# Performance work log

Hardware: AMD Instinct MI355X
Metric: run time of the kernel (lower is better)

Reference implementation:

```python
import jax, jax.numpy as jnp
import numpy as np

LOSS_ALPHA = 0.7  # Config.loss_alpha


def setup_inputs() -> dict:
    key = jax.random.key(0)
    k1, k2, k3 = jax.random.split(key, 3)
    N, D, K = 1024, 256, 65536
    online_emb = jax.random.normal(k1, (N, D), dtype=jnp.float32)
    mom_emb = jax.random.normal(k2, (N, D), dtype=jnp.float32)
    queue = jax.random.normal(k3, (D, K), dtype=jnp.float32)
    temp = jnp.full((1,), 0.07, dtype=jnp.float32)
    return {"online_emb": online_emb, "mom_emb": mom_emb, "queue": queue, "temp": temp}


def _ce_label0(logits):
    # cross-entropy with target class 0 for every row, mean over batch
    return jnp.mean(jax.nn.logsumexp(logits, axis=1) - logits[:, 0])


def reference(online_emb, mom_emb, queue, temp):
    pos_sim = jnp.einsum('nd,nd->n', online_emb, mom_emb)          # [N]
    neg_sim = jnp.einsum('nd,dk->nk', online_emb, queue)           # [N, K]
    logits_raw = jnp.concatenate([pos_sim[:, None], neg_sim], axis=1)  # [N, K+1]
    t = temp[0]
    loss_online = _ce_label0(logits_raw / t)
    loss_momentum = _ce_label0(logits_raw / jax.lax.stop_gradient(t))
    return LOSS_ALPHA * loss_online + (1.0 - LOSS_ALPHA) * loss_momentum
```

## Files before the change

### kernel.cpp

```cpp
#include <hip/hip_runtime.h>
#include <hip/hip_bf16.h>


#define NROWS 1024
#define DDIM  256
#define KQ    65536
#define BN    128
#define NPART 512
#define LN2_F 0.69314718055994531f

typedef short  short8  __attribute__((ext_vector_type(8)));
typedef float  floatx4 __attribute__((ext_vector_type(4)));

__device__ __forceinline__ unsigned short f2bf(float f) {
    unsigned int u = __float_as_uint(f);
    u += 0x7FFFu + ((u >> 16) & 1u);
    return (unsigned short)(u >> 16);
}

#define DPPMOV(x, ctrl) \
    __uint_as_float(__builtin_amdgcn_mov_dpp(__float_as_uint(x), (ctrl), 0xF, 0xF, true))

__device__ __forceinline__ float dpp16_max(float x) {
    x = fmaxf(x, DPPMOV(x, 0xB1));
    x = fmaxf(x, DPPMOV(x, 0x4E));
    x = fmaxf(x, DPPMOV(x, 0x141));
    x = fmaxf(x, DPPMOV(x, 0x140));
    return x;
}
__device__ __forceinline__ float dpp16_sum(float x) {
    x += DPPMOV(x, 0xB1);
    x += DPPMOV(x, 0x4E);
    x += DPPMOV(x, 0x141);
    x += DPPMOV(x, 0x140);
    return x;
}

__global__ __launch_bounds__(256)
void conv_a(const float* __restrict__ A, const float* __restrict__ temp,
            unsigned short* __restrict__ Ab, float* __restrict__ out)
{
    if (blockIdx.x == 0 && threadIdx.x == 0) out[0] = 0.0f;
    const float s = 1.0f / (temp[0] * LN2_F);
    const int i = blockIdx.x * 256 + threadIdx.x;
    const floatx4 v = ((const floatx4*)A)[i];
    ushort4 w;
    w.x = f2bf(v.x * s); w.y = f2bf(v.y * s);
    w.z = f2bf(v.z * s); w.w = f2bf(v.w * s);
    ((ushort4*)Ab)[i] = w;
}

__global__ __launch_bounds__(512, 4)
void gemm_softmax(const unsigned short* __restrict__ Ab,
                  const float* __restrict__ Q,
                  float2* __restrict__ partials)
{
    __shared__ __align__(16) unsigned short Bl[BN * DDIM];

    const int tid  = threadIdx.x;
    const int lane = tid & 63;
    const int wave = tid >> 6;
    const int l15  = lane & 15;
    const int quad = lane >> 4;
    const int nb   = blockIdx.x;
    const int nbase = nb * BN;

    #pragma unroll 1
    for (int iter = 0; iter < 2; ++iter) {
        const int t2 = iter * 512 + tid;
        const int ny = t2 & 31;
        const int ko = t2 >> 5;
        floatx4 v[8];
        #pragma unroll
        for (int j = 0; j < 8; ++j)
            v[j] = __builtin_nontemporal_load(
                       (const floatx4*)(Q + (size_t)(ko * 8 + j) * KQ + nbase + ny * 4));
        #pragma unroll
        for (int i2 = 0; i2 < 4; ++i2) {
            const int n = ny * 4 + i2;
            const int phys = ko ^ (n & 15);
            short8 w;
            #pragma unroll
            for (int j = 0; j < 8; ++j)
                w[j] = (short)f2bf(v[j][i2]);
            *(short8*)&Bl[n * DDIM + phys * 8] = w;
        }
    }
    __syncthreads();

    #pragma unroll 1
    for (int g = 0; g < 4; ++g) {
        const int rowbase = g * 256 + wave * 32;
        const unsigned short* apb = Ab + (size_t)(rowbase + l15) * DDIM + quad * 8;

        floatx4 acc[2][8] = {};
        short8 af[2], bf[8];

        #pragma unroll 1
        for (int s = 0; s < 8; ++s) {
            #pragma unroll
            for (int i = 0; i < 2; ++i)
                af[i] = *(const short8*)(apb + i * 16 * DDIM + s * 32);
            {
                const int vb = l15 * 512 + (((4 * s + quad) ^ l15) * 16);
                #pragma unroll
                for (int j = 0; j < 8; ++j)
                    bf[j] = *(const short8*)((const char*)Bl + vb + j * 8192);
            }
            __builtin_amdgcn_s_setprio(1);
            #pragma unroll
            for (int i = 0; i < 2; ++i)
                #pragma unroll
                for (int j = 0; j < 8; ++j)
                    acc[i][j] = __builtin_amdgcn_mfma_f32_16x16x32_bf16(af[i], bf[j], acc[i][j], 0, 0, 0);
            __builtin_amdgcn_s_setprio(0);
        }

        #pragma unroll
        for (int i = 0; i < 2; ++i) {
            float2 tmp[4];
            #pragma unroll
            for (int r = 0; r < 4; ++r) {
                float mx = acc[i][0][r];
                #pragma unroll
                for (int j = 1; j < 8; ++j) mx = fmaxf(mx, acc[i][j][r]);
                mx = dpp16_max(mx);
                float s2 = 0.f;
                #pragma unroll
                for (int j = 0; j < 8; ++j)
                    s2 += __builtin_amdgcn_exp2f(acc[i][j][r] - mx);
                s2 = dpp16_sum(s2);
                tmp[r] = make_float2(mx, s2);
            }
            if (l15 == 0) {
                const int row = rowbase + i * 16 + quad * 4;
                floatx4* dst = (floatx4*)(partials + (size_t)nb * NROWS + row);
                floatx4 w0 = {tmp[0].x, tmp[0].y, tmp[1].x, tmp[1].y};
                floatx4 w1 = {tmp[2].x, tmp[2].y, tmp[3].x, tmp[3].y};
                __builtin_nontemporal_store(w0, dst);
                __builtin_nontemporal_store(w1, dst + 1);
            }
        }
    }
}

__global__ __launch_bounds__(256)
void finalize_rows(const float2* __restrict__ partials,
                   const float* __restrict__ online,
                   const float* __restrict__ mom,
                   const float* __restrict__ temp,
                   float* __restrict__ out)
{
    const int t = threadIdx.x;
    __shared__ float2 sm[16][17];
    __shared__ float sm_pos[16];

    {
        const float s = 1.0f / (temp[0] * LN2_F);
        const int r2 = t >> 4, c2 = t & 15;
        const float* po = online + (size_t)(blockIdx.x * 16 + r2) * DDIM + c2 * 16;
        const float* pm = mom    + (size_t)(blockIdx.x * 16 + r2) * DDIM + c2 * 16;
        float d = 0.f;
        #pragma unroll
        for (int w = 0; w < 4; ++w) {
            const floatx4 a = *(const floatx4*)(po + w * 4);
            const floatx4 b = *(const floatx4*)(pm + w * 4);
            d += a.x * b.x + a.y * b.y + a.z * b.z + a.w * b.w;
        }
        d = dpp16_sum(d);
        if (c2 == 0) sm_pos[r2] = d * s;
    }

    const int rl  = t & 15;
    const int grp = t >> 4;
    const int row = blockIdx.x * 16 + rl;

    float M = -3.0e38f, S = 0.f;
    #pragma unroll 1
    for (int pb = 0; pb < 32; pb += 8) {
        float2 v[8];
        #pragma unroll
        for (int j = 0; j < 8; ++j)
            v[j] = partials[(size_t)(grp * 32 + pb + j) * NROWS + row];
        #pragma unroll
        for (int j = 0; j < 8; ++j) {
            const float M2 = fmaxf(M, v[j].x);
            S = S * __builtin_amdgcn_exp2f(M - M2) + v[j].y * __builtin_amdgcn_exp2f(v[j].x - M2);
            M = M2;
        }
    }
    sm[grp][rl] = make_float2(M, S);
    __syncthreads();

    if (t < 64) {
        float val = 0.f;
        if (t < 16) {
            float Mm = -3.0e38f, Ss = 0.f;
            #pragma unroll
            for (int g2 = 0; g2 < 16; ++g2) {
                const float2 v = sm[g2][t];
                const float M2 = fmaxf(Mm, v.x);
                Ss = Ss * __builtin_amdgcn_exp2f(Mm - M2) + v.y * __builtin_amdgcn_exp2f(v.x - M2);
                Mm = M2;
            }
            const float p  = sm_pos[t];
            const float M2 = fmaxf(Mm, p);
            const float L  = Ss * __builtin_amdgcn_exp2f(Mm - M2) + __builtin_amdgcn_exp2f(p - M2);
            val = (M2 + __builtin_amdgcn_logf(L) - p) * LN2_F;
        }
        val += __shfl_xor(val, 1, 64);
        val += __shfl_xor(val, 2, 64);
        val += __shfl_xor(val, 4, 64);
        val += __shfl_xor(val, 8, 64);
        val += __shfl_xor(val, 16, 64);
        val += __shfl_xor(val, 32, 64);
        if (t == 0) atomicAdd(out, val * (1.0f / (float)NROWS));
    }
}

extern "C" void kernel_launch(void* const* d_in, const int* in_sizes, int n_in,
                              void* d_out, int out_size, void* d_ws, size_t ws_size,
                              hipStream_t stream)
{
    const float* online = (const float*)d_in[0];
    const float* mom    = (const float*)d_in[1];
    const float* queue  = (const float*)d_in[2];
    const float* temp   = (const float*)d_in[3];
    float* out = (float*)d_out;

    char* ws = (char*)d_ws;
    unsigned short* Ab = (unsigned short*)ws;
    float2* partials   = (float2*)(ws + 524288);

    conv_a<<<256, 256, 0, stream>>>(online, temp, Ab, out);
    gemm_softmax<<<KQ / BN, 512, 0, stream>>>(Ab, queue, partials);
    finalize_rows<<<64, 256, 0, stream>>>(partials, online, mom, temp, out);
}
```

Baseline: 146.6 us.

## Split queue tile staging into two K-halves to overlap load with MFMA

The B tile in LDS is split into two halves along D. The first half is loaded and converted, and the load of the second half is issued before the first compute pass, then written to LDS after the first half's MFMAs for the first row group. The goal is to hide part of the global load latency of the queue tile behind compute instead of stalling all waves before any MFMA. Holding the second-half registers live during compute raises register pressure. The first row group also takes an extra barrier.

Result: slower. 159.0 us (+8.5%).

```diff
diff --git a/kernel.cpp b/kernel.cpp
--- a/kernel.cpp
+++ b/kernel.cpp
@@ -55,7 +55,7 @@
                   const float* __restrict__ Q,
                   float2* __restrict__ partials)
 {
-    __shared__ __align__(16) unsigned short Bl[BN * DDIM];
+    __shared__ __align__(16) unsigned short Bl[2][BN * 128];
 
     const int tid  = threadIdx.x;
     const int lane = tid & 63;
@@ -65,47 +65,47 @@
     const int nb   = blockIdx.x;
     const int nbase = nb * BN;
 
-    #pragma unroll 1
-    for (int iter = 0; iter < 2; ++iter) {
-        const int t2 = iter * 512 + tid;
-        const int ny = t2 & 31;
-        const int ko = t2 >> 5;
-        floatx4 v[8];
+    const int ny = tid & 31;
+    const int ko = tid >> 5;
+
+    {
+        floatx4 v0[8];
         #pragma unroll
         for (int j = 0; j < 8; ++j)
-            v[j] = __builtin_nontemporal_load(
-                       (const floatx4*)(Q + (size_t)(ko * 8 + j) * KQ + nbase + ny * 4));
+            v0[j] = __builtin_nontemporal_load(
+                        (const floatx4*)(Q + (size_t)(ko * 8 + j) * KQ + nbase + ny * 4));
         #pragma unroll
         for (int i2 = 0; i2 < 4; ++i2) {
             const int n = ny * 4 + i2;
             const int phys = ko ^ (n & 15);
             short8 w;
             #pragma unroll
-            for (int j = 0; j < 8; ++j)
-                w[j] = (short)f2bf(v[j][i2]);
-            *(short8*)&Bl[n * DDIM + phys * 8] = w;
-        }
-    }
-    __syncthreads();
-
-    #pragma unroll 1
-    for (int g = 0; g < 4; ++g) {
-        const int rowbase = g * 256 + wave * 32;
-        const unsigned short* apb = Ab + (size_t)(rowbase + l15) * DDIM + quad * 8;
-
-        floatx4 acc[2][8] = {};
-        short8 af[2], bf[8];
-
+            for (int j = 0; j < 8; ++j) w[j] = (short)f2bf(v0[j][i2]);
+            *(short8*)&Bl[0][n * 128 + phys * 8] = w;
+        }
+    }
+    floatx4 sv[8];
+    #pragma unroll
+    for (int j = 0; j < 8; ++j)
+        sv[j] = __builtin_nontemporal_load(
+                    (const floatx4*)(Q + (size_t)(128 + ko * 8 + j) * KQ + nbase + ny * 4));
+
+    asm volatile("s_waitcnt lgkmcnt(0)" ::: "memory");
+    __builtin_amdgcn_s_barrier();
+
+    auto half_steps = [&](floatx4 (&acc)[2][8], const unsigned short* apb,
+                          const char* blc, int af_off) {
         #pragma unroll 1
-        for (int s = 0; s < 8; ++s) {
+        for (int s = 0; s < 4; ++s) {
+            short8 af[2], bf[8];
             #pragma unroll
             for (int i = 0; i < 2; ++i)
-                af[i] = *(const short8*)(apb + i * 16 * DDIM + s * 32);
+                af[i] = *(const short8*)(apb + i * 16 * DDIM + af_off + s * 32);
             {
-                const int vb = l15 * 512 + (((4 * s + quad) ^ l15) * 16);
+                const int vb = l15 * 256 + (((4 * s + quad) ^ l15) * 16);
                 #pragma unroll
                 for (int j = 0; j < 8; ++j)
-                    bf[j] = *(const short8*)((const char*)Bl + vb + j * 8192);
+                    bf[j] = *(const short8*)(blc + vb + j * 4096);
             }
             __builtin_amdgcn_s_setprio(1);
             #pragma unroll
@@ -115,7 +115,9 @@
                     acc[i][j] = __builtin_amdgcn_mfma_f32_16x16x32_bf16(af[i], bf[j], acc[i][j], 0, 0, 0);
             __builtin_amdgcn_s_setprio(0);
         }
-
+    };
+
+    auto epilogue = [&](floatx4 (&acc)[2][8], int rowbase) {
         #pragma unroll
         for (int i = 0; i < 2; ++i) {
             float2 tmp[4];
@@ -141,6 +143,38 @@
                 __builtin_nontemporal_store(w1, dst + 1);
             }
         }
+    };
+
+    {
+        const int rowbase = wave * 32;
+        const unsigned short* apb = Ab + (size_t)(rowbase + l15) * DDIM + quad * 8;
+        floatx4 acc[2][8] = {};
+        half_steps(acc, apb, (const char*)&Bl[0][0], 0);
+
+        #pragma unroll
+        for (int i2 = 0; i2 < 4; ++i2) {
+            const int n = ny * 4 + i2;
+            const int phys = ko ^ (n & 15);
+            short8 w;
+            #pragma unroll
+            for (int j = 0; j < 8; ++j) w[j] = (short)f2bf(sv[j][i2]);
+            *(short8*)&Bl[1][n * 128 + phys * 8] = w;
+        }
+        asm volatile("s_waitcnt lgkmcnt(0)" ::: "memory");
+        __builtin_amdgcn_s_barrier();
+
+        half_steps(acc, apb, (const char*)&Bl[1][0], 128);
+        epilogue(acc, rowbase);
+    }
+
+    #pragma unroll 1
+    for (int g = 1; g < 4; ++g) {
+        const int rowbase = g * 256 + wave * 32;
+        const unsigned short* apb = Ab + (size_t)(rowbase + l15) * DDIM + quad * 8;
+        floatx4 acc[2][8] = {};
+        half_steps(acc, apb, (const char*)&Bl[0][0], 0);
+        half_steps(acc, apb, (const char*)&Bl[1][0], 128);
+        epilogue(acc, rowbase);
     }
 }
 
```
